# Kernel optimization log

Hardware: AMD Instinct MI355X
Metric: run time of the kernel (lower is better)

The kernel has to match this reference:

```python
import jax, jax.numpy as jnp
import numpy as np

EPS = 1e-9
WINDOW = 5
TEMP = 1.0


def _ln(x, g, b):
    m = jnp.mean(x, -1, keepdims=True)
    v = jnp.mean((x - m) ** 2, -1, keepdims=True)
    return (x - m) * jax.lax.rsqrt(v + 1e-5) * g + b


def setup_inputs() -> dict:
    key = jax.random.key(0)
    ks = jax.random.split(key, 20)
    N, S, D, H, W = 32, 512, 256, 1024, WINDOW
    sd = 0.02
    inp = {
        'sequence': jax.random.normal(ks[0], (N, S, D), jnp.float32),
        'input_mask': jnp.ones((N, S, 1), jnp.float32),
        'START': jax.random.normal(ks[1], (D,), jnp.float32),
        'END': jax.random.normal(ks[2], (D,), jnp.float32),
        'yes_t': jax.random.normal(ks[3], (1, 1, D), jnp.float32),
        'no_t': jax.random.normal(ks[4], (1, 1, D), jnp.float32),
        'convW': jax.random.normal(ks[5], (W * D, D), jnp.float32) * sd,
        'convb': jnp.zeros((D,), jnp.float32),
        'scW': jax.random.normal(ks[6], (D, 1), jnp.float32) * sd,
        'scb': jnp.zeros((1,), jnp.float32),
        'itW': jax.random.normal(ks[7], (D, D), jnp.float32) * sd,
        'itb': jnp.zeros((D,), jnp.float32),
        'w1W': jax.random.normal(ks[8], (2 * D, H), jnp.float32) * sd,
        'w1b': jnp.zeros((H,), jnp.float32),
        'w2W': jax.random.normal(ks[9], (H, 4 * D), jnp.float32) * sd,
        'w2b': jnp.zeros((4 * D,), jnp.float32),
        'lng': jnp.ones((D,), jnp.float32),
        'lnb': jnp.zeros((D,), jnp.float32),
        'n_steps': 6,
    }
    return inp


def _forward(sequence, input_mask, START, END, yes_t, no_t, convW, convb, scW, scb,
             itW, itb, w1W, w1b, w2W, w2b, lng, lnb, n_steps):
    N, S, D = sequence.shape
    dt = sequence.dtype
    # ---- augment_sequence: add soft START / END tokens ----
    seq = jnp.concatenate([jnp.broadcast_to(START.reshape(1, 1, D), (N, 1, D)), sequence], 1)
    mask = jnp.concatenate([jnp.ones((N, 1, 1), dt), input_mask], 1)            # (N,S+1,1)
    mask_no_end = jnp.concatenate([mask, jnp.zeros((N, 1, 1), dt)], 1)          # (N,S+2,1)
    mask_yes_end = jnp.concatenate([jnp.ones((N, 1, 1), dt), mask], 1)
    END_mask = mask_yes_end - mask_no_end
    seq = jnp.concatenate([seq, jnp.zeros((N, 1, D), dt)], 1)                   # (N,S+2,D)
    seq = END_mask * END.reshape(1, 1, D) + (1 - END_mask) * seq
    mask = mask_yes_end
    mask_no_start = jnp.concatenate([jnp.zeros((N, 1, 1), dt), mask[:, 1:]], 1)
    S2 = S + 2
    last_token_mask = jnp.concatenate([END_mask[:, 1:], jnp.zeros((N, 1, 1), dt)], 1)
    selp = mask_no_start * mask_no_end * (1.0 - last_token_mask)                # START_END_LAST_PAD_mask

    active = jnp.ones((N, S2, 1), dt) * mask
    ltp = jnp.zeros((N, S2, 1), dt)
    seq = _ln(seq @ itW + itb, lng, lnb) * mask                                 # initial_transform

    def neighbor_probs(active, mask):
        am = jnp.swapaxes(mask, 1, 2)                                           # (N,1,S2)
        ap = jnp.swapaxes(active, 1, 2)
        am2 = jnp.stack([am[:, :, ::-1], am], 1)                                # (N,2,1,S2)
        ap2 = jnp.stack([ap[:, :, ::-1], ap], 1)
        mat = jnp.broadcast_to(ap2, (N, 2, S2, S2)) * am2                       # (N,2,S2,S2)
        right_exist = jnp.triu(mat, 1)
        log_not = jnp.triu(jnp.log(1.0 - right_exist + EPS), 1)
        not_yet = jnp.exp(jnp.cumsum(log_not, -1))
        not_yet = jnp.concatenate([jnp.ones((N, 2, S2, 1), dt), not_yet[..., :-1]], -1)
        rp = right_exist * not_yet * am2
        left = rp[:, 0][:, ::-1, ::-1]                                          # flip dims (1,2)
        right = rp[:, 1]
        return left, right

    for _ in range(n_steps):
        lnp, rnp = neighbor_probs(active, mask)
        tf = ltp * yes_t + (1 - ltp) * no_t
        base = seq + tf
        lk, rk = base, base
        lefts, rights = [], []
        for _k in range(WINDOW // 2):                                           # k-hop soft neighbors
            lk = lnp @ lk
            lefts = [lk] + lefts
            rk = rnp @ rk
            rights = rights + [rk]
        ws = jnp.stack(lefts + [base] + rights, -2)                             # (N,S2,W,D)
        flat = ws.reshape(N, S2, WINDOW * D)
        tsc = (jax.nn.gelu(flat @ convW + convb) @ scW + scb)[..., 0:1] / TEMP
        mx = jnp.maximum(jnp.max(tsc), 0.0)                                     # no-op score is 0
        et = jnp.exp(tsc - mx) * selp
        en = jnp.exp(-mx)
        tp = et / (et + en + EPS)                                               # transition prob
        # ---- composer (gated cell) on (left child, self) ----
        left_child = lnp @ seq
        cc = jnp.concatenate([left_child, seq], -1)
        inter = jax.nn.gelu(cc @ w1W + w1b)
        contents = (inter @ w2W + w2b).reshape(N, S2, 4, D)
        gates = jax.nn.sigmoid(contents[:, :, :3])
        parent = contents[:, :, 3]
        comp = _ln(gates[:, :, 0] * left_child + gates[:, :, 1] * seq + gates[:, :, 2] * parent, lng, lnb)
        seq = (tp * comp + (1 - tp) * seq) * mask
        # left child of a transitioning node becomes inactive
        deact = jnp.einsum('bij,bi->bj', lnp, tp[..., 0])[..., None]
        active = jnp.clip(active * (1.0 - deact), 0.0, 1.0) * mask
        ltp = tp
    return seq


def reference(sequence, input_mask, START, END, yes_t, no_t, convW, convb, scW, scb,
              itW, itb, w1W, w1b, w2W, w2b, lng, lnb, n_steps):
    return _forward(sequence, input_mask, START, END, yes_t, no_t, convW, convb, scW, scb,
                    itW, itb, w1W, w1b, w2W, w2b, lng, lnb, int(n_steps))
```

## Files before the change

### kernel.cpp

```cpp
#include <hip/hip_runtime.h>
#include <math.h>

#define NB 32
#define SS 512
#define S2 514
#define DD 256
#define HH 1024
#define MS (NB*S2)
#define MP 16512
#define EPSF 1e-9f
#define NSTEPS 6
#define NCH 9

typedef unsigned short ushort_t;
typedef __attribute__((ext_vector_type(8))) short short8;
typedef __attribute__((ext_vector_type(4))) float f32x4;

__device__ __forceinline__ float gelu_f(float x){
  float t = tanhf(0.7978845608028654f*(x + 0.044715f*x*x*x));
  return 0.5f*x*(1.f+t);
}
__device__ __forceinline__ float sigmoid_f(float x){ return 1.f/(1.f+expf(-x)); }
__device__ __forceinline__ ushort_t f2bf(float f){
  unsigned u = __float_as_uint(f);
  u += 0x7fffu + ((u>>16)&1u);
  return (ushort_t)(u>>16);
}
__device__ __forceinline__ float bf2f(ushort_t b){
  return __uint_as_float(((unsigned)b)<<16);
}
__device__ __forceinline__ void gload_lds16(const void* g, void* l){
  __builtin_amdgcn_global_load_lds((const __attribute__((address_space(1))) void*)g,
                                   (__attribute__((address_space(3))) void*)l, 16, 0, 0);
}

__global__ __launch_bounds__(256) void k_wt(const float* __restrict__ W, ushort_t* __restrict__ WT,
                                            int K, int N){
  __shared__ float t[64][65];
  int k0 = blockIdx.x*64, n0 = blockIdx.y*64;
  int tx = threadIdx.x & 63, ty = threadIdx.x >> 6;
#pragma unroll
  for (int i=ty;i<64;i+=4) t[i][tx] = W[(size_t)(k0+i)*N + n0 + tx];
  __syncthreads();
#pragma unroll
  for (int i=ty;i<64;i+=4) WT[(size_t)(n0+i)*K + k0 + tx] = f2bf(t[tx][i]);
}

__global__ void k_build_seq0(const float* __restrict__ seq_in, const float* __restrict__ START,
                             const float* __restrict__ END, ushort_t* __restrict__ out){
  int m = blockIdx.x; int d = threadIdx.x;
  int s = m % S2; int b = m / S2;
  float v;
  if (s == 0)        v = START[d];
  else if (s <= SS)  v = seq_in[((size_t)(b*SS + (s-1)))*DD + d];
  else               v = END[d];
  out[(size_t)m*DD + d] = f2bf(v);
}

__global__ void k_init_state(float* __restrict__ ltp, float* __restrict__ act){
  int i = blockIdx.x*256 + threadIdx.x;
  if (i < MS){ ltp[i]=0.f; act[i]=1.f; }
}

template<int ACT, int OUTBF, int SCORE, int NTILE, int DOMAX>
__global__ __launch_bounds__(256) void k_mgemm(const ushort_t* __restrict__ A,
    const ushort_t* __restrict__ BT, const float* __restrict__ bias,
    float* __restrict__ Cf, ushort_t* __restrict__ Cb,
    const float* __restrict__ scW, float* __restrict__ tsc, unsigned* __restrict__ mxp,
    int M, int N, int K)
{
  __shared__ __align__(16) ushort_t Asm[2][128*32];
  __shared__ __align__(16) ushort_t Bsm[2][NTILE*32];
  const int tid = threadIdx.x;
  const int lane = tid & 63, wid = tid >> 6;

  if (DOMAX){
    if (blockIdx.x < 32){
      __shared__ float redm[4];
      float v = 0.f;
      for (int i = blockIdx.x*256 + tid; i < MS; i += 8192) v = fmaxf(v, tsc[i]);
      for (int off=32; off; off>>=1) v = fmaxf(v, __shfl_down(v,off));
      if ((tid&63)==0) redm[tid>>6]=v;
      __syncthreads();
      if (tid==0){
        float r = fmaxf(fmaxf(redm[0],redm[1]),fmaxf(redm[2],redm[3]));
        atomicMax(mxp, __float_as_uint(r));
      }
    }
  }

  const int nwg = gridDim.x, f = blockIdx.x;
  const int q = nwg >> 3, r = nwg & 7;
  const int x = f & 7, jj = f >> 3;
  const int logical = (x < r ? x*(q+1) : r*(q+1) + (x-r)*q) + jj;
  const int NX = N / NTILE;
  const int bx = logical % NX, by = logical / NX;
  const int m0 = by * 128, n0 = bx * NTILE;
  const int MI = (NTILE==128) ? 4 : 2;
  const int wr = (NTILE==128) ? (wid>>1)*64 : wid*32;
  const int wc = (NTILE==128) ? (wid&1)*64  : 0;

  f32x4 acc[4][4];
#pragma unroll
  for (int i=0;i<MI;i++)
#pragma unroll
    for (int j=0;j<4;j++) acc[i][j] = (f32x4){0.f,0.f,0.f,0.f};

  const int srow4 = lane >> 2;
  const int scol = ((((lane&3) - (lane>>3)) & 3) << 3);
  const int rrow = lane & 15, rhi = lane >> 4;

  const int nt = K >> 5;

#define STAGE_T(tt_, bi_)                                                              \
  {                                                                                    \
    const int k0_ = (tt_) << 5;                                                        \
    _Pragma("unroll")                                                                  \
    for (int cc_=0; cc_<2; ++cc_){                                                     \
      int c_ = wid + 4*cc_;                                                            \
      gload_lds16(A + (size_t)(m0 + c_*16 + srow4)*K + k0_ + scol, &Asm[bi_][c_*512]); \
      if (NTILE==128 || cc_==0)                                                        \
        gload_lds16(BT + (size_t)(n0 + c_*16 + srow4)*K + k0_ + scol, &Bsm[bi_][c_*512]); \
    }                                                                                  \
  }

  STAGE_T(0, 0);
  asm volatile("s_waitcnt vmcnt(0)\n\ts_barrier" ::: "memory");

  int cur = 0;
  for (int t=0; t<nt; ++t){
    if (t+1 < nt) STAGE_T(t+1, cur^1);
    short8 a[4], b[4];
#pragma unroll
    for (int i=0;i<MI;i++){
      int ra = wr + i*16 + rrow;
      int sa = ((rhi + (ra>>1)) & 3) << 3;
      a[i] = *reinterpret_cast<const short8*>(&Asm[cur][ra*32 + sa]);
    }
#pragma unroll
    for (int j=0;j<4;j++){
      int rb = wc + j*16 + rrow;
      int sb = ((rhi + (rb>>1)) & 3) << 3;
      b[j] = *reinterpret_cast<const short8*>(&Bsm[cur][rb*32 + sb]);
    }
    __builtin_amdgcn_s_setprio(1);
#pragma unroll
    for (int i=0;i<MI;i++)
#pragma unroll
      for (int j=0;j<4;j++)
        acc[i][j] = __builtin_amdgcn_mfma_f32_16x16x32_bf16(a[i], b[j], acc[i][j], 0,0,0);
    __builtin_amdgcn_s_setprio(0);
    if (t+1 < nt){
      asm volatile("s_waitcnt vmcnt(0)\n\ts_barrier" ::: "memory");
      cur ^= 1;
    }
  }
#undef STAGE_T

  if (SCORE){
#pragma unroll
    for (int i=0;i<MI;i++){
#pragma unroll
      for (int rreg=0;rreg<4;rreg++){
        float rs = 0.f;
#pragma unroll
        for (int j=0;j<4;j++){
          int gn = n0 + wc + j*16 + (lane&15);
          float v = gelu_f(acc[i][j][rreg] + bias[gn]);
          rs += v * scW[gn];
        }
        rs += __shfl_xor(rs,1); rs += __shfl_xor(rs,2);
        rs += __shfl_xor(rs,4); rs += __shfl_xor(rs,8);
        if ((lane&15)==0){
          int gm = m0 + wr + i*16 + (lane>>4)*4 + rreg;
          atomicAdd(&tsc[gm], rs);
        }
      }
    }
  } else {
#pragma unroll
    for (int i=0;i<MI;i++){
#pragma unroll
      for (int rreg=0;rreg<4;rreg++){
        size_t gm = m0 + wr + i*16 + (lane>>4)*4 + rreg;
#pragma unroll
        for (int j=0;j<4;j++){
          int gn = n0 + wc + j*16 + (lane&15);
          float v = acc[i][j][rreg] + bias[gn];
          if (ACT==1) v = gelu_f(v);
          if (OUTBF) Cb[gm*N + gn] = f2bf(v);
          else       Cf[gm*N + gn] = v;
        }
      }
    }
  }
}

__global__ __launch_bounds__(256) void k_ln(const float* __restrict__ x, const float* __restrict__ g,
                                            const float* __restrict__ bta, float* __restrict__ out,
                                            ushort_t* __restrict__ cc){
  __shared__ float red[8];
  int m = blockIdx.x, d = threadIdx.x;
  float v = x[(size_t)m*DD + d];
  float s1 = v, s2 = v*v;
  for (int off=32; off; off>>=1){ s1 += __shfl_down(s1,off); s2 += __shfl_down(s2,off); }
  int wid = d >> 6;
  if ((d&63)==0){ red[wid*2]=s1; red[wid*2+1]=s2; }
  __syncthreads();
  float sum = red[0]+red[2]+red[4]+red[6];
  float sq  = red[1]+red[3]+red[5]+red[7];
  float mean = sum * (1.f/DD);
  float var  = sq  * (1.f/DD) - mean*mean;
  float inv  = rsqrtf(fmaxf(var,0.f) + 1e-5f);
  float o = (v-mean)*inv*g[d] + bta[d];
  out[(size_t)m*DD + d] = o;
  cc[(size_t)m*(2*DD) + DD + d] = f2bf(o);
}

template<int PASS>
__global__ __launch_bounds__(64) void k_scanchunk(
    const ushort_t* __restrict__ ccp, const float* __restrict__ ltpp, const float* __restrict__ actp,
    const float* __restrict__ yes_t, const float* __restrict__ no_t,
    ushort_t* __restrict__ ws5, ushort_t* __restrict__ ccw,
    float* __restrict__ carry, float* __restrict__ scal,
    float* __restrict__ tscp, const float* __restrict__ scb, unsigned* __restrict__ mxp)
{
  __shared__ ushort_t s_sv[66][64];
  __shared__ float s_lt[66], s_ac[66];
  const int b = blockIdx.x, dg = blockIdx.y & 3, ck = blockIdx.y >> 2, dir = blockIdx.z, t = threadIdx.x;
  const size_t mb = (size_t)b*S2;

  if (PASS==0 && dir==0 && dg==0 && ck==0){
    float sbv = scb[0];
    for (int i=t;i<S2;i+=64) tscp[mb+i]=sbv;
    if (b==0 && t==0) *mxp = 0u;
  }

  int st, ln;
  if (dir==0){ st = ck*64; ln = (S2 - st < 64) ? (S2 - st) : 64; }
  else { int hi = (S2-1) - ck*64; st = (hi-63 < 0) ? 0 : hi-63; ln = hi - st + 1; }
  const int lo = st - 1;
  for (int r=0; r<ln+2; ++r){
    int gr = lo + r; gr = gr < 0 ? 0 : (gr > S2-1 ? S2-1 : gr);
    s_sv[r][t] = ccp[(mb+gr)*(2*DD) + DD + (dg<<6) + t];
  }
  for (int r=t; r<ln+2; r+=64){
    int gr = lo + r; gr = gr < 0 ? 0 : (gr > S2-1 ? S2-1 : gr);
    s_lt[r] = ltpp[mb+gr]; s_ac[r] = actp[mb+gr];
  }
  __syncthreads();
  const int d = (dg<<6)+t;
  const float yv = yes_t[d], nv = no_t[d];
  float ci1=0.f, ci2=0.f, cic=0.f;
  const size_t cbase = (((size_t)b*2+dir)*NCH + ck)*3*DD;
  if (PASS==1){
    float s1=0.f, s2=0.f, sc=0.f;
    for (int k=0;k<ck;k++){
      size_t cb2 = (((size_t)b*2+dir)*NCH + k)*3*DD;
      size_t sb = (((size_t)b*2+dir)*NCH + k)*2;
      float Ak = scal[sb], Bk = scal[sb+1];
      float l1 = carry[cb2+d], l2 = carry[cb2+DD+d];
      float ns1 = l1 + Ak*s1;
      float ns2 = l2 + Bk*s1 + Ak*s2;
      if (dir==0){ sc = carry[cb2+2*DD+d] + Ak*sc; }
      s1=ns1; s2=ns2;
    }
    ci1=s1; ci2=s2; cic=sc;
  }
  float A=1.f, Bs=0.f, z1=0.f, z2=0.f, zc=0.f;
  const int pr = (dir==0) ? 0 : (ln+1);
  float svp = bf2f(s_sv[pr][t]); float ltpv = s_lt[pr];
  float pb = svp + ltpv*yv + (1.f-ltpv)*nv, ps = svp, pa = s_ac[pr];
  for (int i=0;i<ln;i++){
    const int r = (dir==0) ? (i+1) : (ln-i);
    const int s = (dir==0) ? (st+i) : (st+ln-1-i);
    float sv = bf2f(s_sv[r][t]); float lt = s_lt[r]; float av = s_ac[r];
    float bse = sv + lt*yv + (1.f-lt)*nv;
    bool upd = (dir==0) ? (s>0) : (s<S2-1);
    if (upd){
      float c = pa, fc = 1.f-c+EPSF;
      z2 = c*z1 + fc*z2;
      z1 = c*pb + fc*z1;
      zc = c*ps + fc*zc;
      Bs = c*A + fc*Bs; A = fc*A;
    }
    if (PASS==1){
      size_t m = mb + s; size_t w5 = m*(5*DD);
      float Z1 = z1 + A*ci1, Z2 = z2 + Bs*ci1 + A*ci2;
      if (dir==0){
        float Zc = zc + A*cic;
        ws5[w5 + d]        = f2bf(Z2);
        ws5[w5 + DD + d]   = f2bf(Z1);
        ws5[w5 + 2*DD + d] = f2bf(bse);
        ccw[m*(2*DD) + d]  = f2bf(Zc);
      } else {
        ws5[w5 + 3*DD + d] = f2bf(Z1);
        ws5[w5 + 4*DD + d] = f2bf(Z2);
      }
    }
    pb=bse; ps=sv; pa=av;
  }
  if (PASS==0){
    carry[cbase+d] = z1; carry[cbase+DD+d] = z2;
    if (dir==0) carry[cbase+2*DD+d] = zc;
    if (dg==0 && t==0){ size_t sb = (((size_t)b*2+dir)*NCH+ck)*2; scal[sb]=A; scal[sb+1]=Bs; }
  }
}

__global__ __launch_bounds__(256) void k_epi(const ushort_t* __restrict__ contents,
     const float* __restrict__ tsc, const unsigned* __restrict__ mx,
     const float* __restrict__ g, const float* __restrict__ bta,
     float* __restrict__ seq, ushort_t* __restrict__ cc, float* __restrict__ ltp){
  __shared__ float red[8];
  int m = blockIdx.x, d = threadIdx.x;
  int s = m % S2;
  float M = __uint_as_float(*mx);
  float sel = (s >= 1 && s <= SS-1) ? 1.f : 0.f;
  float et = expf(tsc[m]-M)*sel;
  float tpv = et/(et+expf(-M)+EPSF);
  if (d==0) ltp[m] = tpv;

  size_t b4 = (size_t)m*HH;
  float lcv = bf2f(cc[(size_t)m*(2*DD) + d]);
  float sv  = seq[(size_t)m*DD+d];
  float g0 = sigmoid_f(bf2f(contents[b4 + d]));
  float g1 = sigmoid_f(bf2f(contents[b4 + DD + d]));
  float g2 = sigmoid_f(bf2f(contents[b4 + 2*DD + d]));
  float pv = bf2f(contents[b4 + 3*DD + d]);
  float xv = g0*lcv + g1*sv + g2*pv;
  float s1=xv, s2=xv*xv;
  for (int off=32; off; off>>=1){ s1 += __shfl_down(s1,off); s2 += __shfl_down(s2,off); }
  int wid = d>>6;
  if ((d&63)==0){ red[wid*2]=s1; red[wid*2+1]=s2; }
  __syncthreads();
  float sum=red[0]+red[2]+red[4]+red[6];
  float sq =red[1]+red[3]+red[5]+red[7];
  float mean = sum*(1.f/DD);
  float var  = sq *(1.f/DD)-mean*mean;
  float inv = rsqrtf(fmaxf(var,0.f)+1e-5f);
  float comp = (xv-mean)*inv*g[d] + bta[d];
  float o = tpv*comp + (1.f-tpv)*sv;
  seq[(size_t)m*DD+d] = o;
  cc[(size_t)m*(2*DD) + DD + d] = f2bf(o);
}

__global__ __launch_bounds__(64) void k_actup(const float* __restrict__ tp, float* __restrict__ act){
  __shared__ float s_a[S2], s_t[S2], s_o[S2];
  int b = blockIdx.x, t = threadIdx.x;
  for (int s=t;s<S2;s+=64){ s_a[s]=act[(size_t)b*S2+s]; s_t[s]=tp[(size_t)b*S2+s]; }
  __syncthreads();
  int hi = (S2-1) - 9*t;
  int lo = hi - 8; if (lo < 0) lo = 0;
  float A=1.f, Bv=0.f;
  if (hi >= 0){
    for (int s=hi; s>=lo; --s){
      float fc = 1.f - s_a[s] + EPSF;
      Bv = s_t[s] + fc*Bv; A = fc*A;
    }
  }
  float Ai=A, Bi=Bv;
  for (int off=1; off<64; off<<=1){
    float Ao = __shfl_up(Ai, off), Bo = __shfl_up(Bi, off);
    if (t >= off){ Bi = Bi + Ai*Bo; Ai = Ai*Ao; }
  }
  float uin = __shfl_up(Bi, 1); if (t==0) uin = 0.f;
  if (hi >= 0){
    float u = uin;
    for (int s=hi; s>=lo; --s){
      float a = s_a[s];
      float na = a*(1.f - a*u);
      s_o[s] = fminf(fmaxf(na,0.f),1.f);
      u = s_t[s] + (1.f - a + EPSF)*u;
    }
  }
  __syncthreads();
  for (int s=t;s<S2;s+=64) act[(size_t)b*S2+s]=s_o[s];
}

extern "C" void kernel_launch(void* const* d_in, const int* in_sizes, int n_in,
                              void* d_out, int out_size, void* d_ws, size_t ws_size,
                              hipStream_t stream){
  const float* seq_in = (const float*)d_in[0];
  const float* START = (const float*)d_in[2];
  const float* END   = (const float*)d_in[3];
  const float* yes_t = (const float*)d_in[4];
  const float* no_t  = (const float*)d_in[5];
  const float* convW = (const float*)d_in[6];
  const float* convb = (const float*)d_in[7];
  const float* scW   = (const float*)d_in[8];
  const float* scb   = (const float*)d_in[9];
  const float* itW   = (const float*)d_in[10];
  const float* itb   = (const float*)d_in[11];
  const float* w1W   = (const float*)d_in[12];
  const float* w1b   = (const float*)d_in[13];
  const float* w2W   = (const float*)d_in[14];
  const float* w2b   = (const float*)d_in[15];
  const float* lng   = (const float*)d_in[16];
  const float* lnb   = (const float*)d_in[17];

  char* p = (char*)d_ws;
  float*    seq  = (float*)p;    p += (size_t)MP*DD*4;
  ushort_t* cc   = (ushort_t*)p; p += (size_t)MP*(2*DD)*2;
  ushort_t* ws5      = (ushort_t*)p;
  ushort_t* contents = (ushort_t*)p;
  float*    preLN    = (float*)p; p += (size_t)MP*2560;
  ushort_t* inter = (ushort_t*)p;
  ushort_t* seq0  = (ushort_t*)p; p += (size_t)MP*2048;
  ushort_t* itWT   = (ushort_t*)p; p += (size_t)256*256*2;
  ushort_t* convWT = (ushort_t*)p; p += (size_t)256*1280*2;
  ushort_t* w1WT   = (ushort_t*)p; p += (size_t)1024*512*2;
  ushort_t* w2WT   = (ushort_t*)p; p += (size_t)1024*1024*2;
  float* ltp = (float*)p; p += (size_t)MS*4;
  float* act = (float*)p; p += (size_t)MS*4;
  float* tsc = (float*)p; p += (size_t)MP*4;
  unsigned* mx = (unsigned*)p; p += 256;
  float* carryL = (float*)p; p += (size_t)NB*2*NCH*3*DD*4;
  float* scal   = (float*)p; p += (size_t)NB*2*NCH*2*4;

  dim3 b256(256), b64(64);

  { dim3 g(256/64, 256/64);   k_wt<<<g, b256, 0, stream>>>(itW,  itWT,  256, 256); }
  { dim3 g(1280/64, 256/64);  k_wt<<<g, b256, 0, stream>>>(convW,convWT,1280,256); }
  { dim3 g(512/64, 1024/64);  k_wt<<<g, b256, 0, stream>>>(w1W,  w1WT,  512, 1024); }
  { dim3 g(1024/64, 1024/64); k_wt<<<g, b256, 0, stream>>>(w2W,  w2WT,  1024,1024); }

  k_build_seq0<<<MS, 256, 0, stream>>>(seq_in, START, END, seq0);
  { int nwg = (256/64)*(MP/128);
    k_mgemm<0,0,0,64,0><<<nwg, b256, 0, stream>>>(seq0, itWT, itb, preLN, nullptr, nullptr, nullptr, nullptr, MP, 256, 256); }
  k_ln<<<MS, 256, 0, stream>>>(preLN, lng, lnb, seq, cc);
  k_init_state<<<(MS+255)/256, 256, 0, stream>>>(ltp, act);

  for (int step=0; step<NSTEPS; ++step){
    { dim3 g(NB, 4*NCH, 2);
      k_scanchunk<0><<<g, b64, 0, stream>>>(cc, ltp, act, yes_t, no_t, ws5, cc, carryL, scal, tsc, scb, mx); }
    { dim3 g(NB, 4*NCH, 2);
      k_scanchunk<1><<<g, b64, 0, stream>>>(cc, ltp, act, yes_t, no_t, ws5, cc, carryL, scal, tsc, scb, mx); }
    { int nwg = (256/64)*(MP/128);
      k_mgemm<0,0,1,64,0><<<nwg, b256, 0, stream>>>(ws5, convWT, convb, nullptr, nullptr, scW, tsc, nullptr, MP, 256, 5*DD); }
    { int nwg = (HH/128)*(MP/128);
      k_mgemm<1,1,0,128,1><<<nwg, b256, 0, stream>>>(cc, w1WT, w1b, nullptr, inter, nullptr, tsc, mx, MP, HH, 2*DD); }
    { int nwg = (HH/128)*(MP/128);
      k_mgemm<0,1,0,128,0><<<nwg, b256, 0, stream>>>(inter, w2WT, w2b, nullptr, contents, nullptr, nullptr, nullptr, MP, HH, HH); }
    k_epi<<<MS, 256, 0, stream>>>(contents, tsc, mx, lng, lnb, seq, cc, ltp);
    k_actup<<<NB, b64, 0, stream>>>(ltp, act);
  }
  hipMemcpyAsync(d_out, seq, (size_t)out_size*sizeof(float), hipMemcpyDeviceToDevice, stream);
}
```

Baseline: 1.293 ms.

## Fuse conv and W1 GEMMs into one launch and merge epilogue with activity update

The conv-score GEMM and the W1 GEMM, which are independent, now share a single grid-partitioned kernel with dynamic shared memory. The global max-score reduction moves into the W2 GEMM. The epilogue is rewritten to handle four rows per block using vectorized loads and wave-level reductions, and it is merged with the activity-update scan, which recomputes transition probabilities from the scores itself. State initialization folds into the sequence-build kernel. Together these cut launch count and let the small conv GEMM overlap with the larger W1 GEMM, at the cost of more complex block dispatch and the W1 path reserving the larger shared-memory footprint for every block.

```diff
diff --git a/kernel.cpp b/kernel.cpp
--- a/kernel.cpp
+++ b/kernel.cpp
@@ -11,6 +11,9 @@
 #define EPSF 1e-9f
 #define NSTEPS 6
 #define NCH 9
+#define CONVN 516
+#define W1N 1032
+#define EPIB 4112
 
 typedef unsigned short ushort_t;
 typedef __attribute__((ext_vector_type(8))) short short8;
@@ -47,7 +50,8 @@
 }
 
 __global__ void k_build_seq0(const float* __restrict__ seq_in, const float* __restrict__ START,
-                             const float* __restrict__ END, ushort_t* __restrict__ out){
+                             const float* __restrict__ END, ushort_t* __restrict__ out,
+                             float* __restrict__ ltp, float* __restrict__ act){
   int m = blockIdx.x; int d = threadIdx.x;
   int s = m % S2; int b = m / S2;
   float v;
@@ -55,41 +59,21 @@
   else if (s <= SS)  v = seq_in[((size_t)(b*SS + (s-1)))*DD + d];
   else               v = END[d];
   out[(size_t)m*DD + d] = f2bf(v);
-}
-
-__global__ void k_init_state(float* __restrict__ ltp, float* __restrict__ act){
-  int i = blockIdx.x*256 + threadIdx.x;
-  if (i < MS){ ltp[i]=0.f; act[i]=1.f; }
-}
-
-template<int ACT, int OUTBF, int SCORE, int NTILE, int DOMAX>
-__global__ __launch_bounds__(256) void k_mgemm(const ushort_t* __restrict__ A,
-    const ushort_t* __restrict__ BT, const float* __restrict__ bias,
-    float* __restrict__ Cf, ushort_t* __restrict__ Cb,
-    const float* __restrict__ scW, float* __restrict__ tsc, unsigned* __restrict__ mxp,
+  if (d == 0){ ltp[m] = 0.f; act[m] = 1.f; }
+}
+
+template<int ACT, int OUTBF, int SCORE, int NTILE>
+__device__ __forceinline__ void gemm_body(int f, int nwg,
+    ushort_t* __restrict__ AsmB, ushort_t* __restrict__ BsmB,
+    const ushort_t* __restrict__ A, const ushort_t* __restrict__ BT,
+    const float* __restrict__ bias, float* __restrict__ Cf, ushort_t* __restrict__ Cb,
+    const float* __restrict__ scW, float* __restrict__ tsc,
     int M, int N, int K)
 {
-  __shared__ __align__(16) ushort_t Asm[2][128*32];
-  __shared__ __align__(16) ushort_t Bsm[2][NTILE*32];
   const int tid = threadIdx.x;
   const int lane = tid & 63, wid = tid >> 6;
-
-  if (DOMAX){
-    if (blockIdx.x < 32){
-      __shared__ float redm[4];
-      float v = 0.f;
-      for (int i = blockIdx.x*256 + tid; i < MS; i += 8192) v = fmaxf(v, tsc[i]);
-      for (int off=32; off; off>>=1) v = fmaxf(v, __shfl_down(v,off));
-      if ((tid&63)==0) redm[tid>>6]=v;
-      __syncthreads();
-      if (tid==0){
-        float r = fmaxf(fmaxf(redm[0],redm[1]),fmaxf(redm[2],redm[3]));
-        atomicMax(mxp, __float_as_uint(r));
-      }
-    }
-  }
-
-  const int nwg = gridDim.x, f = blockIdx.x;
+  const int ASZ = 128*32, BSZ = NTILE*32;
+
   const int q = nwg >> 3, r = nwg & 7;
   const int x = f & 7, jj = f >> 3;
   const int logical = (x < r ? x*(q+1) : r*(q+1) + (x-r)*q) + jj;
@@ -112,16 +96,16 @@
 
   const int nt = K >> 5;
 
-#define STAGE_T(tt_, bi_)                                                              \
-  {                                                                                    \
-    const int k0_ = (tt_) << 5;                                                        \
-    _Pragma("unroll")                                                                  \
-    for (int cc_=0; cc_<2; ++cc_){                                                     \
-      int c_ = wid + 4*cc_;                                                            \
-      gload_lds16(A + (size_t)(m0 + c_*16 + srow4)*K + k0_ + scol, &Asm[bi_][c_*512]); \
-      if (NTILE==128 || cc_==0)                                                        \
-        gload_lds16(BT + (size_t)(n0 + c_*16 + srow4)*K + k0_ + scol, &Bsm[bi_][c_*512]); \
-    }                                                                                  \
+#define STAGE_T(tt_, bi_)                                                                  \
+  {                                                                                        \
+    const int k0_ = (tt_) << 5;                                                            \
+    _Pragma("unroll")                                                                      \
+    for (int cc_=0; cc_<2; ++cc_){                                                         \
+      int c_ = wid + 4*cc_;                                                                \
+      gload_lds16(A + (size_t)(m0 + c_*16 + srow4)*K + k0_ + scol, AsmB + (bi_)*ASZ + c_*512); \
+      if (NTILE==128 || cc_==0)                                                            \
+        gload_lds16(BT + (size_t)(n0 + c_*16 + srow4)*K + k0_ + scol, BsmB + (bi_)*BSZ + c_*512); \
+    }                                                                                      \
   }
 
   STAGE_T(0, 0);
@@ -135,13 +119,13 @@
     for (int i=0;i<MI;i++){
       int ra = wr + i*16 + rrow;
       int sa = ((rhi + (ra>>1)) & 3) << 3;
-      a[i] = *reinterpret_cast<const short8*>(&Asm[cur][ra*32 + sa]);
+      a[i] = *reinterpret_cast<const short8*>(&AsmB[cur*ASZ + ra*32 + sa]);
     }
 #pragma unroll
     for (int j=0;j<4;j++){
       int rb = wc + j*16 + rrow;
       int sb = ((rhi + (rb>>1)) & 3) << 3;
-      b[j] = *reinterpret_cast<const short8*>(&Bsm[cur][rb*32 + sb]);
+      b[j] = *reinterpret_cast<const short8*>(&BsmB[cur*BSZ + rb*32 + sb]);
     }
     __builtin_amdgcn_s_setprio(1);
 #pragma unroll
@@ -193,6 +177,51 @@
         }
       }
     }
+  }
+}
+
+template<int ACT, int OUTBF, int SCORE, int NTILE, int DOMAX>
+__global__ __launch_bounds__(256) void k_mgemm(const ushort_t* __restrict__ A,
+    const ushort_t* __restrict__ BT, const float* __restrict__ bias,
+    float* __restrict__ Cf, ushort_t* __restrict__ Cb,
+    const float* __restrict__ scW, float* __restrict__ tsc, unsigned* __restrict__ mxp,
+    int M, int N, int K)
+{
+  __shared__ __align__(16) ushort_t Asm[2*128*32];
+  __shared__ __align__(16) ushort_t Bsm[2*NTILE*32];
+  if (DOMAX){
+    if (blockIdx.x < 32){
+      __shared__ float redm[4];
+      float v = 0.f;
+      for (int i = blockIdx.x*256 + threadIdx.x; i < MS; i += 8192) v = fmaxf(v, tsc[i]);
+      for (int off=32; off; off>>=1) v = fmaxf(v, __shfl_down(v,off));
+      if ((threadIdx.x&63)==0) redm[threadIdx.x>>6]=v;
+      __syncthreads();
+      if (threadIdx.x==0){
+        float r = fmaxf(fmaxf(redm[0],redm[1]),fmaxf(redm[2],redm[3]));
+        atomicMax(mxp, __float_as_uint(r));
+      }
+    }
+  }
+  gemm_body<ACT,OUTBF,SCORE,NTILE>(blockIdx.x, gridDim.x, Asm, Bsm,
+                                   A, BT, bias, Cf, Cb, scW, tsc, M, N, K);
+}
+
+__global__ __launch_bounds__(256) void k_convw1(
+    const ushort_t* __restrict__ ws5, const ushort_t* __restrict__ convWT,
+    const float* __restrict__ convb, const float* __restrict__ scW, float* __restrict__ tsc,
+    const ushort_t* __restrict__ cc, const ushort_t* __restrict__ w1WT,
+    const float* __restrict__ w1b, ushort_t* __restrict__ inter, int M)
+{
+  extern __shared__ __align__(16) ushort_t dsm[];
+  ushort_t* AsmB = dsm;
+  ushort_t* BsmB = dsm + 2*128*32;
+  if (blockIdx.x < CONVN){
+    gemm_body<0,0,1,64>(blockIdx.x, CONVN, AsmB, BsmB,
+                        ws5, convWT, convb, nullptr, nullptr, scW, tsc, M, 256, 5*DD);
+  } else {
+    gemm_body<1,1,0,128>(blockIdx.x - CONVN, W1N, AsmB, BsmB,
+                         cc, w1WT, w1b, nullptr, inter, nullptr, nullptr, M, HH, 2*DD);
   }
 }
 
@@ -307,74 +336,100 @@
   }
 }
 
-__global__ __launch_bounds__(256) void k_epi(const ushort_t* __restrict__ contents,
+__global__ __launch_bounds__(256) void k_epiact(const ushort_t* __restrict__ contents,
      const float* __restrict__ tsc, const unsigned* __restrict__ mx,
      const float* __restrict__ g, const float* __restrict__ bta,
-     float* __restrict__ seq, ushort_t* __restrict__ cc, float* __restrict__ ltp){
-  __shared__ float red[8];
-  int m = blockIdx.x, d = threadIdx.x;
-  int s = m % S2;
-  float M = __uint_as_float(*mx);
-  float sel = (s >= 1 && s <= SS-1) ? 1.f : 0.f;
-  float et = expf(tsc[m]-M)*sel;
-  float tpv = et/(et+expf(-M)+EPSF);
-  if (d==0) ltp[m] = tpv;
-
-  size_t b4 = (size_t)m*HH;
-  float lcv = bf2f(cc[(size_t)m*(2*DD) + d]);
-  float sv  = seq[(size_t)m*DD+d];
-  float g0 = sigmoid_f(bf2f(contents[b4 + d]));
-  float g1 = sigmoid_f(bf2f(contents[b4 + DD + d]));
-  float g2 = sigmoid_f(bf2f(contents[b4 + 2*DD + d]));
-  float pv = bf2f(contents[b4 + 3*DD + d]);
-  float xv = g0*lcv + g1*sv + g2*pv;
-  float s1=xv, s2=xv*xv;
-  for (int off=32; off; off>>=1){ s1 += __shfl_down(s1,off); s2 += __shfl_down(s2,off); }
-  int wid = d>>6;
-  if ((d&63)==0){ red[wid*2]=s1; red[wid*2+1]=s2; }
-  __syncthreads();
-  float sum=red[0]+red[2]+red[4]+red[6];
-  float sq =red[1]+red[3]+red[5]+red[7];
-  float mean = sum*(1.f/DD);
-  float var  = sq *(1.f/DD)-mean*mean;
-  float inv = rsqrtf(fmaxf(var,0.f)+1e-5f);
-  float comp = (xv-mean)*inv*g[d] + bta[d];
-  float o = tpv*comp + (1.f-tpv)*sv;
-  seq[(size_t)m*DD+d] = o;
-  cc[(size_t)m*(2*DD) + DD + d] = f2bf(o);
-}
-
-__global__ __launch_bounds__(64) void k_actup(const float* __restrict__ tp, float* __restrict__ act){
+     float* __restrict__ seq, ushort_t* __restrict__ cc, float* __restrict__ ltp,
+     float* __restrict__ act)
+{
   __shared__ float s_a[S2], s_t[S2], s_o[S2];
-  int b = blockIdx.x, t = threadIdx.x;
-  for (int s=t;s<S2;s+=64){ s_a[s]=act[(size_t)b*S2+s]; s_t[s]=tp[(size_t)b*S2+s]; }
-  __syncthreads();
-  int hi = (S2-1) - 9*t;
-  int lo = hi - 8; if (lo < 0) lo = 0;
-  float A=1.f, Bv=0.f;
-  if (hi >= 0){
-    for (int s=hi; s>=lo; --s){
-      float fc = 1.f - s_a[s] + EPSF;
-      Bv = s_t[s] + fc*Bv; A = fc*A;
-    }
-  }
-  float Ai=A, Bi=Bv;
-  for (int off=1; off<64; off<<=1){
-    float Ao = __shfl_up(Ai, off), Bo = __shfl_up(Bi, off);
-    if (t >= off){ Bi = Bi + Ai*Bo; Ai = Ai*Ao; }
-  }
-  float uin = __shfl_up(Bi, 1); if (t==0) uin = 0.f;
-  if (hi >= 0){
-    float u = uin;
-    for (int s=hi; s>=lo; --s){
-      float a = s_a[s];
-      float na = a*(1.f - a*u);
-      s_o[s] = fminf(fmaxf(na,0.f),1.f);
-      u = s_t[s] + (1.f - a + EPSF)*u;
-    }
-  }
-  __syncthreads();
-  for (int s=t;s<S2;s+=64) act[(size_t)b*S2+s]=s_o[s];
+  const float M_ = __uint_as_float(*mx);
+  const float en = expf(-M_);
+  if (blockIdx.x < EPIB){
+    const int wid = threadIdx.x >> 6, lane = threadIdx.x & 63;
+    const int m = blockIdx.x*4 + wid;
+    const int s = m % S2;
+    float sel = (s >= 1 && s <= SS-1) ? 1.f : 0.f;
+    float et = expf(tsc[m]-M_)*sel;
+    float tpv = et/(et+en+EPSF);
+    if (lane==0) ltp[m] = tpv;
+
+    const int d0 = lane*4;
+    float4 sv4 = *reinterpret_cast<const float4*>(&seq[(size_t)m*DD + d0]);
+    ushort4 lc4 = *reinterpret_cast<const ushort4*>(&cc[(size_t)m*(2*DD) + d0]);
+    size_t b4 = (size_t)m*HH;
+    ushort4 c0 = *reinterpret_cast<const ushort4*>(&contents[b4 + 0*DD + d0]);
+    ushort4 c1 = *reinterpret_cast<const ushort4*>(&contents[b4 + 1*DD + d0]);
+    ushort4 c2 = *reinterpret_cast<const ushort4*>(&contents[b4 + 2*DD + d0]);
+    ushort4 c3 = *reinterpret_cast<const ushort4*>(&contents[b4 + 3*DD + d0]);
+    float svv[4] = {sv4.x, sv4.y, sv4.z, sv4.w};
+    ushort_t lcs[4] = {lc4.x, lc4.y, lc4.z, lc4.w};
+    ushort_t g0s[4] = {c0.x, c0.y, c0.z, c0.w};
+    ushort_t g1s[4] = {c1.x, c1.y, c1.z, c1.w};
+    ushort_t g2s[4] = {c2.x, c2.y, c2.z, c2.w};
+    ushort_t pvs[4] = {c3.x, c3.y, c3.z, c3.w};
+    float xv[4]; float s1 = 0.f, s2 = 0.f;
+#pragma unroll
+    for (int j=0;j<4;j++){
+      float x = sigmoid_f(bf2f(g0s[j]))*bf2f(lcs[j])
+              + sigmoid_f(bf2f(g1s[j]))*svv[j]
+              + sigmoid_f(bf2f(g2s[j]))*bf2f(pvs[j]);
+      xv[j] = x; s1 += x; s2 += x*x;
+    }
+    for (int off=1; off<64; off<<=1){ s1 += __shfl_xor(s1,off); s2 += __shfl_xor(s2,off); }
+    float mean = s1*(1.f/DD);
+    float var  = s2*(1.f/DD) - mean*mean;
+    float inv  = rsqrtf(fmaxf(var,0.f)+1e-5f);
+    float4 so; ushort4 co;
+    float oo[4];
+#pragma unroll
+    for (int j=0;j<4;j++){
+      float comp = (xv[j]-mean)*inv*g[d0+j] + bta[d0+j];
+      oo[j] = tpv*comp + (1.f-tpv)*svv[j];
+    }
+    so.x=oo[0]; so.y=oo[1]; so.z=oo[2]; so.w=oo[3];
+    co.x=f2bf(oo[0]); co.y=f2bf(oo[1]); co.z=f2bf(oo[2]); co.w=f2bf(oo[3]);
+    *reinterpret_cast<float4*>(&seq[(size_t)m*DD + d0]) = so;
+    *reinterpret_cast<ushort4*>(&cc[(size_t)m*(2*DD) + DD + d0]) = co;
+  } else {
+    const int b = blockIdx.x - EPIB;
+    const int t = threadIdx.x;
+    for (int s=t; s<S2; s+=256){
+      float sel = (s >= 1 && s <= SS-1) ? 1.f : 0.f;
+      float et = expf(tsc[(size_t)b*S2+s]-M_)*sel;
+      s_t[s] = et/(et+en+EPSF);
+      s_a[s] = act[(size_t)b*S2+s];
+    }
+    __syncthreads();
+    if (t < 64){
+      int hi = (S2-1) - 9*t;
+      int lo = hi - 8; if (lo < 0) lo = 0;
+      float A=1.f, Bv=0.f;
+      if (hi >= 0){
+        for (int s=hi; s>=lo; --s){
+          float fc = 1.f - s_a[s] + EPSF;
+          Bv = s_t[s] + fc*Bv; A = fc*A;
+        }
+      }
+      float Ai=A, Bi=Bv;
+      for (int off=1; off<64; off<<=1){
+        float Ao = __shfl_up(Ai, off), Bo = __shfl_up(Bi, off);
+        if (t >= off){ Bi = Bi + Ai*Bo; Ai = Ai*Ao; }
+      }
+      float uin = __shfl_up(Bi, 1); if (t==0) uin = 0.f;
+      if (hi >= 0){
+        float u = uin;
+        for (int s=hi; s>=lo; --s){
+          float a = s_a[s];
+          float na = a*(1.f - a*u);
+          s_o[s] = fminf(fmaxf(na,0.f),1.f);
+          u = s_t[s] + (1.f - a + EPSF)*u;
+        }
+      }
+    }
+    __syncthreads();
+    for (int s=t; s<S2; s+=256) act[(size_t)b*S2+s]=s_o[s];
+  }
 }
 
 extern "C" void kernel_launch(void* const* d_in, const int* in_sizes, int n_in,
@@ -424,25 +479,19 @@
   { dim3 g(512/64, 1024/64);  k_wt<<<g, b256, 0, stream>>>(w1W,  w1WT,  512, 1024); }
   { dim3 g(1024/64, 1024/64); k_wt<<<g, b256, 0, stream>>>(w2W,  w2WT,  1024,1024); }
 
-  k_build_seq0<<<MS, 256, 0, stream>>>(seq_in, START, END, seq0);
-  { int nwg = (256/64)*(MP/128);
-    k_mgemm<0,0,0,64,0><<<nwg, b256, 0, stream>>>(seq0, itWT, itb, preLN, nullptr, nullptr, nullptr, nullptr, MP, 256, 256); }
+  k_build_seq0<<<MS, 256, 0, stream>>>(seq_in, START, END, seq0, ltp, act);
+  k_mgemm<0,0,0,64,0><<<CONVN, b256, 0, stream>>>(seq0, itWT, itb, preLN, nullptr, nullptr, nullptr, nullptr, MP, 256, 256);
   k_ln<<<MS, 256, 0, stream>>>(preLN, lng, lnb, seq, cc);
-  k_init_state<<<(MS+255)/256, 256, 0, stream>>>(ltp, act);
 
   for (int step=0; step<NSTEPS; ++step){
     { dim3 g(NB, 4*NCH, 2);
       k_scanchunk<0><<<g, b64, 0, stream>>>(cc, ltp, act, yes_t, no_t, ws5, cc, carryL, scal, tsc, scb, mx); }
     { dim3 g(NB, 4*NCH, 2);
       k_scanchunk<1><<<g, b64, 0, stream>>>(cc, ltp, act, yes_t, no_t, ws5, cc, carryL, scal, tsc, scb, mx); }
-    { int nwg = (256/64)*(MP/128);
-      k_mgemm<0,0,1,64,0><<<nwg, b256, 0, stream>>>(ws5, convWT, convb, nullptr, nullptr, scW, tsc, nullptr, MP, 256, 5*DD); }
-    { int nwg = (HH/128)*(MP/128);
-      k_mgemm<1,1,0,128,1><<<nwg, b256, 0, stream>>>(cc, w1WT, w1b, nullptr, inter, nullptr, tsc, mx, MP, HH, 2*DD); }
-    { int nwg = (HH/128)*(MP/128);
-      k_mgemm<0,1,0,128,0><<<nwg, b256, 0, stream>>>(inter, w2WT, w2b, nullptr, contents, nullptr, nullptr, nullptr, MP, HH, HH); }
-    k_epi<<<MS, 256, 0, stream>>>(contents, tsc, mx, lng, lnb, seq, cc, ltp);
-    k_actup<<<NB, b64, 0, stream>>>(ltp, act);
+    k_convw1<<<CONVN + W1N, b256, 32768, stream>>>(ws5, convWT, convb, scW, tsc,
+                                                   cc, w1WT, w1b, inter, MP);
+    k_mgemm<0,1,0,128,1><<<W1N, b256, 0, stream>>>(inter, w2WT, w2b, nullptr, contents, nullptr, tsc, mx, MP, HH, HH);
+    k_epiact<<<EPIB + NB, b256, 0, stream>>>(contents, tsc, mx, lng, lnb, seq, cc, ltp, act);
   }
   hipMemcpyAsync(d_out, seq, (size_t)out_size*sizeof(float), hipMemcpyDeviceToDevice, stream);
 }
```

Result: faster. 1.135 ms (-12.2%).
